# Optimization experiments

Hardware: AMD Instinct MI355X
Metric: run time of the kernel (lower is better)

Reference implementation:

```python
import jax, jax.numpy as jnp
import numpy as np

HIDDEN = 2048
N_HEADS = 32
N_KV_HEADS = 8
HEAD_DIM = HIDDEN // N_HEADS  # 64
N_REP = N_HEADS // N_KV_HEADS  # 4
ROPE_THETA = 10000.0


def setup_inputs() -> dict:
    key = jax.random.key(0)
    ks = jax.random.split(key, 6)
    B, S = 1, 2048
    scale = 0.02
    return {
        "hidden_states": jax.random.normal(ks[0], (B, S, HIDDEN), dtype=jnp.float32),
        "Wq": jax.random.normal(ks[1], (HIDDEN, N_HEADS * HEAD_DIM), dtype=jnp.float32) * scale,
        "Wk": jax.random.normal(ks[2], (HIDDEN, N_KV_HEADS * HEAD_DIM), dtype=jnp.float32) * scale,
        "Wv": jax.random.normal(ks[3], (HIDDEN, N_KV_HEADS * HEAD_DIM), dtype=jnp.float32) * scale,
        "Wo": jax.random.normal(ks[4], (HIDDEN, HIDDEN), dtype=jnp.float32) * scale,
        "position_ids": jnp.arange(S, dtype=jnp.int64 if jax.config.jax_enable_x64 else jnp.int32)[None, :],
    }


def _rope_cos_sin(position_ids, dtype):
    # inv_freq: [head_dim//2]
    inv_freq = 1.0 / (ROPE_THETA ** (jnp.arange(0, HEAD_DIM, 2, dtype=jnp.float32) / HEAD_DIM))
    # freqs: [B, S, head_dim//2]
    freqs = position_ids.astype(jnp.float32)[:, :, None] * inv_freq[None, None, :]
    emb = jnp.concatenate([freqs, freqs], axis=-1)  # [B, S, head_dim]
    return jnp.cos(emb).astype(dtype), jnp.sin(emb).astype(dtype)


def _rotate_half(x):
    x1, x2 = jnp.split(x, 2, axis=-1)
    return jnp.concatenate([-x2, x1], axis=-1)


def reference(hidden_states, Wq, Wk, Wv, Wo, position_ids):
    B, S, _ = hidden_states.shape
    # projections -> [B, H, S, D]
    q = (hidden_states @ Wq).reshape(B, S, N_HEADS, HEAD_DIM).transpose(0, 2, 1, 3)
    k = (hidden_states @ Wk).reshape(B, S, N_KV_HEADS, HEAD_DIM).transpose(0, 2, 1, 3)
    v = (hidden_states @ Wv).reshape(B, S, N_KV_HEADS, HEAD_DIM).transpose(0, 2, 1, 3)

    cos, sin = _rope_cos_sin(position_ids, hidden_states.dtype)
    cos = cos[:, None, :, :]  # [B,1,S,D]
    sin = sin[:, None, :, :]
    q = q * cos + _rotate_half(q) * sin
    k = k * cos + _rotate_half(k) * sin

    # GQA: expand kv heads
    k = jnp.repeat(k, N_REP, axis=1)  # [B, H, S, D]
    v = jnp.repeat(v, N_REP, axis=1)

    scores = jnp.einsum("bhqd,bhkd->bhqk", q, k) / np.sqrt(HEAD_DIM).astype(np.float32)
    # additive causal mask
    causal = jnp.tril(jnp.ones((S, S), dtype=bool))
    scores = jnp.where(causal[None, None, :, :], scores, jnp.finfo(jnp.float32).min)
    attn = jax.nn.softmax(scores.astype(jnp.float32), axis=-1).astype(q.dtype)

    out = jnp.einsum("bhqk,bhkd->bhqd", attn, v)  # [B,H,S,D]
    out = out.transpose(0, 2, 1, 3).reshape(B, S, HIDDEN)
    return out @ Wo
```

## Files before the change

### kernel.cpp

```cpp
#include <hip/hip_runtime.h>
#include <stdint.h>

typedef __attribute__((ext_vector_type(8))) short short8;
typedef __attribute__((ext_vector_type(4))) float floatx4;
typedef __attribute__((ext_vector_type(16))) float floatx16;

__device__ __forceinline__ float b2f(unsigned short u) {
    union { unsigned int i; float f; } x; x.i = ((unsigned int)u) << 16; return x.f;
}
__device__ __forceinline__ unsigned short f2b(float f) {
    unsigned int x = __float_as_uint(f);
    return (unsigned short)((x + 0x7FFFu + ((x >> 16) & 1u)) >> 16);
}
__device__ __forceinline__ unsigned int cvt_pk_bf16(float lo, float hi) {
    unsigned int r;
    asm("v_cvt_pk_bf16_f32 %0, %1, %2" : "=v"(r) : "v"(lo), "v"(hi));
    return r;
}
__device__ __forceinline__ float exp2_(float x) {
    float r;
    asm("v_exp_f32 %0, %1" : "=v"(r) : "v"(x));
    return r;
}

__device__ __forceinline__ void gload_lds16(const void* g, void* l) {
    __builtin_amdgcn_global_load_lds((const __attribute__((address_space(1))) unsigned int*)g,
                                     (__attribute__((address_space(3))) unsigned int*)l, 16, 0, 0);
}

__global__ __launch_bounds__(256)
void prep_kernel(const float* __restrict__ Wq, const float* __restrict__ Wk,
                 const float* __restrict__ Wv, const float* __restrict__ Wo,
                 const float* __restrict__ hs,
                 unsigned short* __restrict__ Wqkv, unsigned short* __restrict__ WoT,
                 unsigned short* __restrict__ hs_b) {
    __shared__ float tile[64][65];
    int b = blockIdx.x;
    if (b >= 2560) {
        int i = ((b - 2560) * 256 + threadIdx.x) * 4;
        float4 v = *reinterpret_cast<const float4*>(hs + i);
        hs_b[i + 0] = f2b(v.x);
        hs_b[i + 1] = f2b(v.y);
        hs_b[i + 2] = f2b(v.z);
        hs_b[i + 3] = f2b(v.w);
        return;
    }
    const float* in;
    unsigned short* out;
    int bx, by, ld_in, ld_out;
    if (b < 1024) {
        in = Wq; out = Wqkv; bx = b & 31; by = b >> 5; ld_in = 2048; ld_out = 2048;
    } else if (b < 1280) {
        int c = b - 1024;
        in = Wk; out = Wqkv + (size_t)2048 * 2048; bx = c & 7; by = c >> 3; ld_in = 512; ld_out = 2048;
    } else if (b < 1536) {
        int c = b - 1280;
        in = Wv; out = Wqkv + (size_t)2560 * 2048; bx = c & 7; by = c >> 3; ld_in = 512; ld_out = 2048;
    } else {
        int c = b - 1536;
        in = Wo; out = WoT; bx = c & 31; by = c >> 5; ld_in = 2048; ld_out = 2048;
    }
    int tx = threadIdx.x & 63, ty = threadIdx.x >> 6;
    int c0 = bx * 64, r0 = by * 64;
    #pragma unroll
    for (int i = 0; i < 64; i += 4)
        tile[ty + i][tx] = in[(size_t)(r0 + ty + i) * ld_in + c0 + tx];
    __syncthreads();
    #pragma unroll
    for (int i = 0; i < 64; i += 4)
        out[(size_t)(c0 + ty + i) * ld_out + r0 + tx] = f2b(tile[tx][ty + i]);
}

__global__ void transpose_bf16(const unsigned short* __restrict__ in, unsigned short* __restrict__ out,
                               int ld_in, int ld_out) {
    __shared__ float tile[64][65];
    int tx = threadIdx.x & 63, ty = threadIdx.x >> 6;
    int c0 = blockIdx.x * 64, r0 = blockIdx.y * 64;
    #pragma unroll
    for (int i = 0; i < 64; i += 4)
        tile[ty + i][tx] = b2f(in[(size_t)(r0 + ty + i) * ld_in + c0 + tx]);
    __syncthreads();
    #pragma unroll
    for (int i = 0; i < 64; i += 4)
        out[(size_t)(c0 + ty + i) * ld_out + r0 + tx] = f2b(tile[tx][ty + i]);
}

template<int OF32>
__global__ __launch_bounds__(256)
void gemm64x128(const unsigned short* __restrict__ A, const unsigned short* __restrict__ BT,
                void* __restrict__ Cout, int M, int N, int K) {
    __shared__ __align__(16) unsigned short As[2][64 * 64];
    __shared__ __align__(16) unsigned short Bs[2][128 * 64];
    int tid = threadIdx.x;
    int l = tid & 63, w = tid >> 6;
    int lr = l & 15, lg = l >> 4;

    int gx = gridDim.x;
    int nwg = gx * gridDim.y;
    int flat = blockIdx.y * gx + blockIdx.x;
    int q8 = nwg >> 3;
    int f2 = (flat & 7) * q8 + (flat >> 3);
    int bx = f2 % gx, by = f2 / gx;
    int nb = bx * 128, mb = by * 64;

    floatx4 acc[4][2];
    #pragma unroll
    for (int m = 0; m < 4; ++m)
        #pragma unroll
        for (int f = 0; f < 2; ++f) acc[m][f] = (floatx4)(0.f);

    int ca1 = tid + 256;
    int ra0 = tid >> 3, ja0 = (tid & 7) ^ (ra0 & 7);
    int ra1 = ca1 >> 3, ja1 = (ca1 & 7) ^ (ra1 & 7);
    const unsigned short* Ag0 = A + (size_t)(mb + ra0) * K + ja0 * 8;
    const unsigned short* Ag1 = A + (size_t)(mb + ra1) * K + ja1 * 8;
    const unsigned short* Bg[4];
    #pragma unroll
    for (int i = 0; i < 4; ++i) {
        int c = tid + 256 * i;
        int r = c >> 3, j = (c & 7) ^ (r & 7);
        Bg[i] = BT + (size_t)(nb + r) * K + j * 8;
    }

    auto stage = [&](int buf, int kb) {
        gload_lds16(Ag0 + kb, &As[buf][tid * 8]);
        gload_lds16(Ag1 + kb, &As[buf][ca1 * 8]);
        #pragma unroll
        for (int i = 0; i < 4; ++i)
            gload_lds16(Bg[i] + kb, &Bs[buf][(tid + 256 * i) * 8]);
    };

    int nsteps = K >> 6;
    stage(0, 0);
    for (int it = 0; it < nsteps; ++it) {
        int nxt = (it + 1 < nsteps) ? it + 1 : it;
        stage((it + 1) & 1, nxt * 64);
        asm volatile("s_waitcnt vmcnt(6)" ::: "memory");
        __builtin_amdgcn_s_barrier();
        __builtin_amdgcn_sched_barrier(0);

        const unsigned short* Ab = As[it & 1];
        const unsigned short* Bb = Bs[it & 1];
        #pragma unroll
        for (int kh = 0; kh < 2; ++kh) {
            int sl = ((kh * 4 + lg) ^ (lr & 7)) * 8;
            short8 af[4], bf[2];
            #pragma unroll
            for (int m = 0; m < 4; ++m)
                af[m] = *reinterpret_cast<const short8*>(Ab + (m * 16 + lr) * 64 + sl);
            #pragma unroll
            for (int f = 0; f < 2; ++f)
                bf[f] = *reinterpret_cast<const short8*>(Bb + (w * 32 + f * 16 + lr) * 64 + sl);
            #pragma unroll
            for (int m = 0; m < 4; ++m)
                #pragma unroll
                for (int f = 0; f < 2; ++f)
                    acc[m][f] = __builtin_amdgcn_mfma_f32_16x16x32_bf16(af[m], bf[f], acc[m][f], 0, 0, 0);
        }
        __builtin_amdgcn_sched_barrier(0);
        __builtin_amdgcn_s_barrier();
    }
    asm volatile("s_waitcnt vmcnt(0)" ::: "memory");

    #pragma unroll
    for (int m = 0; m < 4; ++m) {
        int orow = mb + m * 16 + lg * 4;
        #pragma unroll
        for (int f = 0; f < 2; ++f) {
            int ocol = nb + w * 32 + f * 16 + lr;
            #pragma unroll
            for (int r = 0; r < 4; ++r) {
                if (OF32)
                    ((float*)Cout)[(size_t)(orow + r) * N + ocol] = acc[m][f][r];
                else
                    ((unsigned short*)Cout)[(size_t)(orow + r) * N + ocol] = f2b(acc[m][f][r]);
            }
        }
    }
}

__global__ void rope_kernel(unsigned short* __restrict__ qkv, const int* __restrict__ pos_ids) {
    int idx = blockIdx.x * blockDim.x + threadIdx.x;
    int i = idx & 31;
    int hh = (idx >> 5) % 40;
    int s = idx / 1280;
    unsigned short* p;
    float scale;
    if (hh < 32) {
        p = qkv + (size_t)s * 3072 + hh * 64;
        scale = 0.18033688011112042f;
    } else {
        p = qkv + (size_t)s * 3072 + 2048 + (hh - 32) * 64;
        scale = 1.0f;
    }
    float x1 = b2f(p[i]), x2 = b2f(p[i + 32]);
    float pos = (float)pos_ids[s];
    float inv = exp2f(-0.41524101186092029f * (float)i);
    float a = pos * inv;
    float sn, cs;
    __sincosf(a, &sn, &cs);
    p[i]      = f2b((x1 * cs - x2 * sn) * scale);
    p[i + 32] = f2b((x2 * cs + x1 * sn) * scale);
}

__global__ __launch_bounds__(128, 2)
void attn_kernel(const unsigned short* __restrict__ QKV,
                 const unsigned short* __restrict__ VT,
                 unsigned short* __restrict__ O) {
    const int S = 2048, LDQ = 3072, HID = 2048;
    __shared__ __align__(16) char smem[17664];
    unsigned short* KlBase = (unsigned short*)smem;
    float* Ms = (float*)smem;

    int tid = threadIdx.x;
    int l = tid & 63, w = tid >> 6;
    int lq = l & 31, hl = l >> 5;
    int b = blockIdx.x;
    int h = b & 31;
    int pi = b >> 5;
    int bH = 63 - pi, bL = pi;
    int nH = (bH >> 1) + 1;
    int kvh = h >> 2;
    int qH = bH * 32 + lq;
    int qL = bL * 32 + lq;

    const unsigned short* Kg = QKV + 2048 + kvh * 64;
    const unsigned short* Vr0 = VT + (size_t)(kvh * 64 + lq) * S + hl * 8;
    const unsigned short* Vr1 = VT + (size_t)(kvh * 64 + 32 + lq) * S + hl * 8;

    auto stageK = [&](int buf, int c0w) {
        unsigned short* Kl = KlBase + (buf * 2 + w) * 2048;
        #pragma unroll
        for (int i = 0; i < 4; ++i) {
            int c = l + 64 * i;
            int kr = c >> 3, ks = (c & 7) ^ (kr & 7);
            gload_lds16(Kg + (size_t)(c0w + kr) * LDQ + ks * 8, &Kl[c * 8]);
        }
    };

    auto process = [&](int buf, int c0w, const short8* qf, int qrow, bool diag,
                       float& m, float& lsum, floatx16* acc,
                       short8 v00, short8 v01, short8 v10, short8 v11) {
        const unsigned short* Kb = KlBase + (buf * 2 + w) * 2048;
        floatx16 st = (floatx16)(0.f);
        __builtin_amdgcn_s_setprio(1);
        #pragma unroll
        for (int dc = 0; dc < 4; ++dc) {
            short8 kf = *reinterpret_cast<const short8*>(
                Kb + lq * 64 + (((dc * 2 + hl) ^ (lq & 7)) * 8));
            st = __builtin_amdgcn_mfma_f32_32x32x16_bf16(kf, qf[dc], st, 0, 0, 0);
        }
        __builtin_amdgcn_s_setprio(0);
        if (diag) {
            #pragma unroll
            for (int r = 0; r < 16; ++r) {
                int key = c0w + (r & 3) + 8 * (r >> 2) + 4 * hl;
                if (key > qrow) st[r] = -1e30f;
            }
        }
        float t0 = fmaxf(fmaxf(st[0], st[1]), fmaxf(st[2], st[3]));
        float t1 = fmaxf(fmaxf(st[4], st[5]), fmaxf(st[6], st[7]));
        float t2 = fmaxf(fmaxf(st[8], st[9]), fmaxf(st[10], st[11]));
        float t3 = fmaxf(fmaxf(st[12], st[13]), fmaxf(st[14], st[15]));
        float tm = fmaxf(fmaxf(t0, t1), fmaxf(t2, t3));
        tm = fmaxf(tm, __shfl_xor(tm, 32));
        if (!__all(tm <= m + 11.5f)) {
            float mn = fmaxf(m, tm);
            float al = exp2_(m - mn);
            lsum *= al;
            acc[0] *= al;
            acc[1] *= al;
            m = mn;
        }
        float p[16];
        #pragma unroll
        for (int r = 0; r < 16; ++r) p[r] = exp2_(st[r] - m);
        float s0 = (p[0] + p[1]) + (p[2] + p[3]);
        float s1 = (p[4] + p[5]) + (p[6] + p[7]);
        float s2 = (p[8] + p[9]) + (p[10] + p[11]);
        float s3 = (p[12] + p[13]) + (p[14] + p[15]);
        float rs = (s0 + s1) + (s2 + s3);
        rs += __shfl_xor(rs, 32);
        lsum += rs;
        unsigned int u[4][2];
        #pragma unroll
        for (int B2 = 0; B2 < 4; ++B2) {
            u[B2][0] = cvt_pk_bf16(p[B2 * 4 + 0], p[B2 * 4 + 1]);
            u[B2][1] = cvt_pk_bf16(p[B2 * 4 + 2], p[B2 * 4 + 3]);
        }
        asm volatile("s_waitcnt vmcnt(4)" ::: "memory");
        #pragma unroll
        for (int kc = 0; kc < 2; ++kc) {
            unsigned int o0 = u[2 * kc][0],     o1 = u[2 * kc][1];
            unsigned int e0 = u[2 * kc + 1][0], e1 = u[2 * kc + 1][1];
            unsigned int t0x = (unsigned int)__shfl((int)o0, l ^ 32);
            unsigned int t1x = (unsigned int)__shfl((int)o1, l ^ 32);
            unsigned int s0p = (unsigned int)__shfl((int)e0, l ^ 32);
            unsigned int s1p = (unsigned int)__shfl((int)e1, l ^ 32);
            union { unsigned int uu[4]; short8 s8; } pf;
            pf.uu[0] = hl ? s0p : o0;
            pf.uu[1] = hl ? s1p : o1;
            pf.uu[2] = hl ? e0 : t0x;
            pf.uu[3] = hl ? e1 : t1x;
            __builtin_amdgcn_s_setprio(1);
            acc[0] = __builtin_amdgcn_mfma_f32_32x32x16_bf16(kc ? v01 : v00, pf.s8, acc[0], 0, 0, 0);
            acc[1] = __builtin_amdgcn_mfma_f32_32x32x16_bf16(kc ? v11 : v10, pf.s8, acc[1], 0, 0, 0);
            __builtin_amdgcn_s_setprio(0);
        }
    };

    short8 qfH[4];
    {
        const unsigned short* Qr = QKV + (size_t)qH * LDQ + h * 64;
        #pragma unroll
        for (int c = 0; c < 4; ++c)
            qfH[c] = *reinterpret_cast<const short8*>(Qr + c * 16 + hl * 8);
    }
    floatx16 accH[2];
    accH[0] = (floatx16)(0.f); accH[1] = (floatx16)(0.f);
    float mH = -1e30f, lH = 0.f;

    stageK(0, w * 32);
    for (int j = 0; j < nH; ++j) {
        int c0w = j * 64 + w * 32;
        short8 v00 = *reinterpret_cast<const short8*>(Vr0 + c0w);
        short8 v01 = *reinterpret_cast<const short8*>(Vr0 + c0w + 16);
        short8 v10 = *reinterpret_cast<const short8*>(Vr1 + c0w);
        short8 v11 = *reinterpret_cast<const short8*>(Vr1 + c0w + 16);
        __builtin_amdgcn_sched_barrier(0);
        int jn = j + 1;
        int tn = (jn < nH) ? jn : 0;
        stageK(jn & 1, tn * 64 + w * 32);
        asm volatile("s_waitcnt vmcnt(8)" ::: "memory");
        __builtin_amdgcn_sched_barrier(0);
        process(j & 1, c0w, qfH, qH, j == nH - 1, mH, lH, accH, v00, v01, v10, v11);
    }

    short8 qfL[4];
    {
        const unsigned short* Qr = QKV + (size_t)qL * LDQ + h * 64;
        #pragma unroll
        for (int c = 0; c < 4; ++c)
            qfL[c] = *reinterpret_cast<const short8*>(Qr + c * 16 + hl * 8);
    }
    floatx16 accL[2];
    accL[0] = (floatx16)(0.f); accL[1] = (floatx16)(0.f);
    float mL = -1e30f, lL = 0.f;

    for (int j = nH; j < 33; ++j) {
        int cur = j - nH;
        int c0w = cur * 64 + w * 32;
        short8 v00 = *reinterpret_cast<const short8*>(Vr0 + c0w);
        short8 v01 = *reinterpret_cast<const short8*>(Vr0 + c0w + 16);
        short8 v10 = *reinterpret_cast<const short8*>(Vr1 + c0w);
        short8 v11 = *reinterpret_cast<const short8*>(Vr1 + c0w + 16);
        __builtin_amdgcn_sched_barrier(0);
        int jn = j + 1;
        int tn = (jn < 33) ? jn - nH : cur;
        stageK(jn & 1, tn * 64 + w * 32);
        asm volatile("s_waitcnt vmcnt(8)" ::: "memory");
        __builtin_amdgcn_sched_barrier(0);
        process(j & 1, c0w, qfL, qL, j == 32, mL, lL, accL, v00, v01, v10, v11);
    }
    asm volatile("s_waitcnt vmcnt(0)" ::: "memory");
    __syncthreads();

    if (w == 1) {
        Ms[l * 69 + 0] = mH; Ms[l * 69 + 1] = lH;
        Ms[l * 69 + 2] = mL; Ms[l * 69 + 3] = lL;
        #pragma unroll
        for (int d = 0; d < 2; ++d)
            #pragma unroll
            for (int r = 0; r < 16; ++r) {
                Ms[l * 69 + 4 + d * 16 + r]  = accH[d][r];
                Ms[l * 69 + 36 + d * 16 + r] = accL[d][r];
            }
    }
    __syncthreads();
    if (w == 0) {
        #pragma unroll
        for (int band = 0; band < 2; ++band) {
            float m0 = band ? mL : mH;
            float l0 = band ? lL : lH;
            const floatx16* acc = band ? accL : accH;
            int moff = band ? 2 : 0;
            int aoff = band ? 36 : 4;
            int qrow = band ? qL : qH;
            float m1 = Ms[l * 69 + moff], l1 = Ms[l * 69 + moff + 1];
            float mm = fmaxf(m0, m1);
            float a0 = exp2_(m0 - mm), a1 = exp2_(m1 - mm);
            float inv = 1.0f / (l0 * a0 + l1 * a1);
            a0 *= inv; a1 *= inv;
            unsigned short* Op = O + (size_t)qrow * HID + h * 64 + hl * 4;
            #pragma unroll
            for (int d = 0; d < 2; ++d)
                #pragma unroll
                for (int g4 = 0; g4 < 4; ++g4) {
                    float v0 = acc[d][g4 * 4 + 0] * a0 + Ms[l * 69 + aoff + d * 16 + g4 * 4 + 0] * a1;
                    float v1 = acc[d][g4 * 4 + 1] * a0 + Ms[l * 69 + aoff + d * 16 + g4 * 4 + 1] * a1;
                    float v2 = acc[d][g4 * 4 + 2] * a0 + Ms[l * 69 + aoff + d * 16 + g4 * 4 + 2] * a1;
                    float v3 = acc[d][g4 * 4 + 3] * a0 + Ms[l * 69 + aoff + d * 16 + g4 * 4 + 3] * a1;
                    unsigned long long pk = (unsigned long long)cvt_pk_bf16(v0, v1)
                                          | ((unsigned long long)cvt_pk_bf16(v2, v3) << 32);
                    *reinterpret_cast<unsigned long long*>(Op + d * 32 + g4 * 8) = pk;
                }
        }
    }
}

extern "C" void kernel_launch(void* const* d_in, const int* in_sizes, int n_in,
                              void* d_out, int out_size, void* d_ws, size_t ws_size,
                              hipStream_t stream) {
    const int S = 2048, HID = 2048, KVD = 512, NQKV = 3072;
    const float* hs = (const float*)d_in[0];
    const float* Wq = (const float*)d_in[1];
    const float* Wk = (const float*)d_in[2];
    const float* Wv = (const float*)d_in[3];
    const float* Wo = (const float*)d_in[4];
    const int* pos  = (const int*)d_in[5];

    char* base = (char*)d_ws;
    auto alloc = [&](size_t bytes) {
        char* r = base;
        base += (bytes + 255) & ~(size_t)255;
        return r;
    };
    unsigned short* hs_b     = (unsigned short*)alloc((size_t)S * HID * 2);
    unsigned short* Wqkv     = (unsigned short*)alloc((size_t)NQKV * HID * 2);
    unsigned short* WoT      = (unsigned short*)alloc((size_t)HID * HID * 2);
    unsigned short* qkv      = (unsigned short*)alloc((size_t)S * NQKV * 2);
    unsigned short* vT       = (unsigned short*)alloc((size_t)KVD * S * 2);
    unsigned short* attn_out = (unsigned short*)alloc((size_t)S * HID * 2);

    prep_kernel<<<6656, 256, 0, stream>>>(Wq, Wk, Wv, Wo, hs, Wqkv, WoT, hs_b);

    gemm64x128<0><<<dim3(NQKV / 128, S / 64), 256, 0, stream>>>(hs_b, Wqkv, qkv, S, NQKV, HID);

    rope_kernel<<<10240, 256, 0, stream>>>(qkv, pos);

    transpose_bf16<<<dim3(KVD / 64, S / 64), 256, 0, stream>>>(qkv + 2560, vT, NQKV, S);

    attn_kernel<<<1024, 128, 0, stream>>>(qkv, vT, attn_out);

    gemm64x128<1><<<dim3(HID / 128, S / 64), 256, 0, stream>>>(attn_out, WoT, (float*)d_out, S, HID, HID);
}
```

Measured before the change: 137.1 us.

## Drop paired causal bands and LDS K staging; load K fragments directly to registers

Each attention block previously handled a heavy and a light causal query band together for load balance, staging K tiles through LDS with async loads. Now each block handles one 32-row band and 2048 blocks are launched, with blocks ordered heaviest-first. K fragments are double-buffered in registers and loaded straight from global memory, which removes the LDS staging and the second accumulator set. This cuts LDS use and register pressure, but it depends on the hardware scheduler for load balance and reads K with less coalescing.

```diff
diff --git a/kernel.cpp b/kernel.cpp
--- a/kernel.cpp
+++ b/kernel.cpp
@@ -208,48 +208,43 @@
                  const unsigned short* __restrict__ VT,
                  unsigned short* __restrict__ O) {
     const int S = 2048, LDQ = 3072, HID = 2048;
-    __shared__ __align__(16) char smem[17664];
-    unsigned short* KlBase = (unsigned short*)smem;
-    float* Ms = (float*)smem;
+    __shared__ float Ms[64 * 36];
 
     int tid = threadIdx.x;
     int l = tid & 63, w = tid >> 6;
     int lq = l & 31, hl = l >> 5;
     int b = blockIdx.x;
     int h = b & 31;
-    int pi = b >> 5;
-    int bH = 63 - pi, bL = pi;
-    int nH = (bH >> 1) + 1;
+    int band = 63 - (b >> 5);
+    int nT = (band >> 1) + 1;
     int kvh = h >> 2;
-    int qH = bH * 32 + lq;
-    int qL = bL * 32 + lq;
-
-    const unsigned short* Kg = QKV + 2048 + kvh * 64;
+    int qrow = band * 32 + lq;
+
+    short8 qf[4];
+    {
+        const unsigned short* Qr = QKV + (size_t)qrow * LDQ + h * 64;
+        #pragma unroll
+        for (int c = 0; c < 4; ++c)
+            qf[c] = *reinterpret_cast<const short8*>(Qr + c * 16 + hl * 8);
+    }
+
+    const unsigned short* Kp = QKV + 2048 + (size_t)kvh * 64 + hl * 8
+                             + (size_t)(w * 32 + lq) * LDQ;
+    const size_t KSTEP = (size_t)64 * LDQ;
     const unsigned short* Vr0 = VT + (size_t)(kvh * 64 + lq) * S + hl * 8;
     const unsigned short* Vr1 = VT + (size_t)(kvh * 64 + 32 + lq) * S + hl * 8;
 
-    auto stageK = [&](int buf, int c0w) {
-        unsigned short* Kl = KlBase + (buf * 2 + w) * 2048;
-        #pragma unroll
-        for (int i = 0; i < 4; ++i) {
-            int c = l + 64 * i;
-            int kr = c >> 3, ks = (c & 7) ^ (kr & 7);
-            gload_lds16(Kg + (size_t)(c0w + kr) * LDQ + ks * 8, &Kl[c * 8]);
-        }
-    };
-
-    auto process = [&](int buf, int c0w, const short8* qf, int qrow, bool diag,
-                       float& m, float& lsum, floatx16* acc,
+    floatx16 acc[2];
+    acc[0] = (floatx16)(0.f); acc[1] = (floatx16)(0.f);
+    float m_run = -1e30f, l_run = 0.f;
+
+    auto process = [&](const short8* kf, int c0w, bool diag,
                        short8 v00, short8 v01, short8 v10, short8 v11) {
-        const unsigned short* Kb = KlBase + (buf * 2 + w) * 2048;
         floatx16 st = (floatx16)(0.f);
         __builtin_amdgcn_s_setprio(1);
         #pragma unroll
-        for (int dc = 0; dc < 4; ++dc) {
-            short8 kf = *reinterpret_cast<const short8*>(
-                Kb + lq * 64 + (((dc * 2 + hl) ^ (lq & 7)) * 8));
-            st = __builtin_amdgcn_mfma_f32_32x32x16_bf16(kf, qf[dc], st, 0, 0, 0);
-        }
+        for (int dc = 0; dc < 4; ++dc)
+            st = __builtin_amdgcn_mfma_f32_32x32x16_bf16(kf[dc], qf[dc], st, 0, 0, 0);
         __builtin_amdgcn_s_setprio(0);
         if (diag) {
             #pragma unroll
@@ -264,24 +259,24 @@
         float t3 = fmaxf(fmaxf(st[12], st[13]), fmaxf(st[14], st[15]));
         float tm = fmaxf(fmaxf(t0, t1), fmaxf(t2, t3));
         tm = fmaxf(tm, __shfl_xor(tm, 32));
-        if (!__all(tm <= m + 11.5f)) {
-            float mn = fmaxf(m, tm);
-            float al = exp2_(m - mn);
-            lsum *= al;
+        if (!__all(tm <= m_run + 11.5f)) {
+            float mn = fmaxf(m_run, tm);
+            float al = exp2_(m_run - mn);
+            l_run *= al;
             acc[0] *= al;
             acc[1] *= al;
-            m = mn;
+            m_run = mn;
         }
         float p[16];
         #pragma unroll
-        for (int r = 0; r < 16; ++r) p[r] = exp2_(st[r] - m);
+        for (int r = 0; r < 16; ++r) p[r] = exp2_(st[r] - m_run);
         float s0 = (p[0] + p[1]) + (p[2] + p[3]);
         float s1 = (p[4] + p[5]) + (p[6] + p[7]);
         float s2 = (p[8] + p[9]) + (p[10] + p[11]);
         float s3 = (p[12] + p[13]) + (p[14] + p[15]);
         float rs = (s0 + s1) + (s2 + s3);
         rs += __shfl_xor(rs, 32);
-        lsum += rs;
+        l_run += rs;
         unsigned int u[4][2];
         #pragma unroll
         for (int B2 = 0; B2 < 4; ++B2) {
@@ -309,102 +304,82 @@
         }
     };
 
-    short8 qfH[4];
-    {
-        const unsigned short* Qr = QKV + (size_t)qH * LDQ + h * 64;
-        #pragma unroll
-        for (int c = 0; c < 4; ++c)
-            qfH[c] = *reinterpret_cast<const short8*>(Qr + c * 16 + hl * 8);
-    }
-    floatx16 accH[2];
-    accH[0] = (floatx16)(0.f); accH[1] = (floatx16)(0.f);
-    float mH = -1e30f, lH = 0.f;
-
-    stageK(0, w * 32);
-    for (int j = 0; j < nH; ++j) {
-        int c0w = j * 64 + w * 32;
-        short8 v00 = *reinterpret_cast<const short8*>(Vr0 + c0w);
-        short8 v01 = *reinterpret_cast<const short8*>(Vr0 + c0w + 16);
-        short8 v10 = *reinterpret_cast<const short8*>(Vr1 + c0w);
-        short8 v11 = *reinterpret_cast<const short8*>(Vr1 + c0w + 16);
-        __builtin_amdgcn_sched_barrier(0);
-        int jn = j + 1;
-        int tn = (jn < nH) ? jn : 0;
-        stageK(jn & 1, tn * 64 + w * 32);
-        asm volatile("s_waitcnt vmcnt(8)" ::: "memory");
-        __builtin_amdgcn_sched_barrier(0);
-        process(j & 1, c0w, qfH, qH, j == nH - 1, mH, lH, accH, v00, v01, v10, v11);
-    }
-
-    short8 qfL[4];
-    {
-        const unsigned short* Qr = QKV + (size_t)qL * LDQ + h * 64;
-        #pragma unroll
-        for (int c = 0; c < 4; ++c)
-            qfL[c] = *reinterpret_cast<const short8*>(Qr + c * 16 + hl * 8);
-    }
-    floatx16 accL[2];
-    accL[0] = (floatx16)(0.f); accL[1] = (floatx16)(0.f);
-    float mL = -1e30f, lL = 0.f;
-
-    for (int j = nH; j < 33; ++j) {
-        int cur = j - nH;
-        int c0w = cur * 64 + w * 32;
-        short8 v00 = *reinterpret_cast<const short8*>(Vr0 + c0w);
-        short8 v01 = *reinterpret_cast<const short8*>(Vr0 + c0w + 16);
-        short8 v10 = *reinterpret_cast<const short8*>(Vr1 + c0w);
-        short8 v11 = *reinterpret_cast<const short8*>(Vr1 + c0w + 16);
-        __builtin_amdgcn_sched_barrier(0);
-        int jn = j + 1;
-        int tn = (jn < 33) ? jn - nH : cur;
-        stageK(jn & 1, tn * 64 + w * 32);
-        asm volatile("s_waitcnt vmcnt(8)" ::: "memory");
-        __builtin_amdgcn_sched_barrier(0);
-        process(j & 1, c0w, qfL, qL, j == 32, mL, lL, accL, v00, v01, v10, v11);
+    short8 kA[4], kB[4];
+    #pragma unroll
+    for (int dc = 0; dc < 4; ++dc)
+        kA[dc] = *reinterpret_cast<const short8*>(Kp + dc * 16);
+
+    int j = 0;
+    while (true) {
+        {
+            int c0w = j * 64 + w * 32;
+            bool last = (j == nT - 1);
+            short8 v00 = *reinterpret_cast<const short8*>(Vr0 + c0w);
+            short8 v01 = *reinterpret_cast<const short8*>(Vr0 + c0w + 16);
+            short8 v10 = *reinterpret_cast<const short8*>(Vr1 + c0w);
+            short8 v11 = *reinterpret_cast<const short8*>(Vr1 + c0w + 16);
+            __builtin_amdgcn_sched_barrier(0);
+            const unsigned short* Kn = last ? Kp : Kp + KSTEP;
+            #pragma unroll
+            for (int dc = 0; dc < 4; ++dc)
+                kB[dc] = *reinterpret_cast<const short8*>(Kn + dc * 16);
+            asm volatile("s_waitcnt vmcnt(8)" ::: "memory");
+            __builtin_amdgcn_sched_barrier(0);
+            process(kA, c0w, last, v00, v01, v10, v11);
+            if (last) break;
+            ++j; Kp = Kn;
+        }
+        {
+            int c0w = j * 64 + w * 32;
+            bool last = (j == nT - 1);
+            short8 v00 = *reinterpret_cast<const short8*>(Vr0 + c0w);
+            short8 v01 = *reinterpret_cast<const short8*>(Vr0 + c0w + 16);
+            short8 v10 = *reinterpret_cast<const short8*>(Vr1 + c0w);
+            short8 v11 = *reinterpret_cast<const short8*>(Vr1 + c0w + 16);
+            __builtin_amdgcn_sched_barrier(0);
+            const unsigned short* Kn = last ? Kp : Kp + KSTEP;
+            #pragma unroll
+            for (int dc = 0; dc < 4; ++dc)
+                kA[dc] = *reinterpret_cast<const short8*>(Kn + dc * 16);
+            asm volatile("s_waitcnt vmcnt(8)" ::: "memory");
+            __builtin_amdgcn_sched_barrier(0);
+            process(kB, c0w, last, v00, v01, v10, v11);
+            if (last) break;
+            ++j; Kp = Kn;
+        }
     }
     asm volatile("s_waitcnt vmcnt(0)" ::: "memory");
     __syncthreads();
 
     if (w == 1) {
-        Ms[l * 69 + 0] = mH; Ms[l * 69 + 1] = lH;
-        Ms[l * 69 + 2] = mL; Ms[l * 69 + 3] = lL;
+        Ms[l * 36 + 0] = m_run;
+        Ms[l * 36 + 1] = l_run;
         #pragma unroll
         for (int d = 0; d < 2; ++d)
             #pragma unroll
-            for (int r = 0; r < 16; ++r) {
-                Ms[l * 69 + 4 + d * 16 + r]  = accH[d][r];
-                Ms[l * 69 + 36 + d * 16 + r] = accL[d][r];
-            }
+            for (int r = 0; r < 16; ++r)
+                Ms[l * 36 + 2 + d * 16 + r] = acc[d][r];
     }
     __syncthreads();
     if (w == 0) {
-        #pragma unroll
-        for (int band = 0; band < 2; ++band) {
-            float m0 = band ? mL : mH;
-            float l0 = band ? lL : lH;
-            const floatx16* acc = band ? accL : accH;
-            int moff = band ? 2 : 0;
-            int aoff = band ? 36 : 4;
-            int qrow = band ? qL : qH;
-            float m1 = Ms[l * 69 + moff], l1 = Ms[l * 69 + moff + 1];
-            float mm = fmaxf(m0, m1);
-            float a0 = exp2_(m0 - mm), a1 = exp2_(m1 - mm);
-            float inv = 1.0f / (l0 * a0 + l1 * a1);
-            a0 *= inv; a1 *= inv;
-            unsigned short* Op = O + (size_t)qrow * HID + h * 64 + hl * 4;
-            #pragma unroll
-            for (int d = 0; d < 2; ++d)
-                #pragma unroll
-                for (int g4 = 0; g4 < 4; ++g4) {
-                    float v0 = acc[d][g4 * 4 + 0] * a0 + Ms[l * 69 + aoff + d * 16 + g4 * 4 + 0] * a1;
-                    float v1 = acc[d][g4 * 4 + 1] * a0 + Ms[l * 69 + aoff + d * 16 + g4 * 4 + 1] * a1;
-                    float v2 = acc[d][g4 * 4 + 2] * a0 + Ms[l * 69 + aoff + d * 16 + g4 * 4 + 2] * a1;
-                    float v3 = acc[d][g4 * 4 + 3] * a0 + Ms[l * 69 + aoff + d * 16 + g4 * 4 + 3] * a1;
-                    unsigned long long pk = (unsigned long long)cvt_pk_bf16(v0, v1)
-                                          | ((unsigned long long)cvt_pk_bf16(v2, v3) << 32);
-                    *reinterpret_cast<unsigned long long*>(Op + d * 32 + g4 * 8) = pk;
-                }
-        }
+        float m1 = Ms[l * 36 + 0], l1 = Ms[l * 36 + 1];
+        float mm = fmaxf(m_run, m1);
+        float a0 = exp2_(m_run - mm), a1 = exp2_(m1 - mm);
+        float inv = 1.0f / (l_run * a0 + l1 * a1);
+        a0 *= inv; a1 *= inv;
+        unsigned short* Op = O + (size_t)qrow * HID + h * 64 + hl * 4;
+        #pragma unroll
+        for (int d = 0; d < 2; ++d)
+            #pragma unroll
+            for (int g4 = 0; g4 < 4; ++g4) {
+                float v0 = acc[d][g4 * 4 + 0] * a0 + Ms[l * 36 + 2 + d * 16 + g4 * 4 + 0] * a1;
+                float v1 = acc[d][g4 * 4 + 1] * a0 + Ms[l * 36 + 2 + d * 16 + g4 * 4 + 1] * a1;
+                float v2 = acc[d][g4 * 4 + 2] * a0 + Ms[l * 36 + 2 + d * 16 + g4 * 4 + 2] * a1;
+                float v3 = acc[d][g4 * 4 + 3] * a0 + Ms[l * 36 + 2 + d * 16 + g4 * 4 + 3] * a1;
+                unsigned long long pk = (unsigned long long)cvt_pk_bf16(v0, v1)
+                                      | ((unsigned long long)cvt_pk_bf16(v2, v3) << 32);
+                *reinterpret_cast<unsigned long long*>(Op + d * 32 + g4 * 8) = pk;
+            }
     }
 }
 
@@ -440,7 +415,7 @@
 
     transpose_bf16<<<dim3(KVD / 64, S / 64), 256, 0, stream>>>(qkv + 2560, vT, NQKV, S);
 
-    attn_kernel<<<1024, 128, 0, stream>>>(qkv, vT, attn_out);
+    attn_kernel<<<2048, 128, 0, stream>>>(qkv, vT, attn_out);
 
     gemm64x128<1><<<dim3(HID / 128, S / 64), 256, 0, stream>>>(attn_out, WoT, (float*)d_out, S, HID, HID);
 }
```

New measurement: 160.3 us. 1.17x slower.
